# Kernel optimization log

Hardware: AMD Instinct MI355X
Metric: run time of the kernel (lower is better)

## Reference

```python
import jax, jax.numpy as jnp
import numpy as np
from jax import lax

B, C_VIS, C_GRAPH, C_OUT, H, W, K = 8, 256, 256, 256, 96, 96, 3


def conv2d(x, w, b):
    # x: [B,Cin,H,W], w: [Cout,Cin,K,K], SAME padding (pad = K//2)
    y = lax.conv_general_dilated(x, w, window_strides=(1, 1), padding='SAME',
                                 dimension_numbers=('NCHW', 'OIHW', 'NCHW'))
    return y + b[None, :, None, None]


def setup_inputs() -> dict:
    key = jax.random.key(0)
    ks = jax.random.split(key, 12)
    scale_v = 1.0 / np.sqrt(C_VIS * K * K)
    scale_g = 1.0 / np.sqrt(C_GRAPH * K * K)
    scale_o = 1.0 / np.sqrt(C_OUT * K * K)
    return {
        'feats': jax.random.normal(ks[0], (B, C_VIS, H, W), jnp.float32),
        'graph_feature': jax.random.normal(ks[1], (B, C_GRAPH, H, W), jnp.float32),
        'wq': jax.random.normal(ks[2], (C_OUT, C_GRAPH, K, K), jnp.float32) * scale_g,
        'bq': jax.random.normal(ks[3], (C_OUT,), jnp.float32) * 0.01,
        'wk': jax.random.normal(ks[4], (C_OUT, C_VIS, K, K), jnp.float32) * scale_v,
        'bk': jax.random.normal(ks[5], (C_OUT,), jnp.float32) * 0.01,
        'wv': jax.random.normal(ks[6], (C_OUT, C_VIS, K, K), jnp.float32) * scale_v,
        'bv': jax.random.normal(ks[7], (C_OUT,), jnp.float32) * 0.01,
        'wo': jax.random.normal(ks[8], (C_OUT, C_OUT, K, K), jnp.float32) * scale_o,
        'bo': jax.random.normal(ks[9], (C_OUT,), jnp.float32) * 0.01,
    }


def reference(feats, graph_feature, wq, bq, wk, bk, wv, bv, wo, bo):
    q = conv2d(graph_feature, wq, bq)  # [B,C,H,W]
    k = conv2d(feats, wk, bk)          # [B,C,H,W]
    v = conv2d(feats, wv, bv)          # [B,C,H,W]
    # attention over rows: attn[b,c,i,j] = sum_w q[b,c,i,w] * k[b,c,j,w]
    scale = 1.0 / jnp.sqrt(jnp.asarray(k.shape[-1], q.dtype))
    attn = jnp.einsum('bchw,bcgw->bchg', q, k) * scale  # [B,C,H,H]
    attn = jax.nn.softmax(attn, axis=-1)
    fused = jnp.einsum('bchg,bcgw->bchw', attn, v)      # [B,C,H,W]
    return conv2d(fused, wo, bo)
```

## Files before the change

kernel.cpp:

```cpp
#include <hip/hip_runtime.h>
#include <hip/hip_bf16.h>

constexpr int BATCH = 8;
constexpr int CH    = 256;
constexpr int H     = 96;
constexpr int W     = 96;
constexpr int HW    = H * W;
constexpr long PLANE_ELEMS = (long)BATCH * CH * HW;
constexpr int PAD   = 98;

typedef short  bf16x8_t  __attribute__((ext_vector_type(8)));
typedef float  f32x4_t   __attribute__((ext_vector_type(4)));
typedef float  f32x16_t  __attribute__((ext_vector_type(16)));

__device__ inline uint pk2_bf16(float a, float b) {
  ushort lo = __bfloat16_as_ushort(__float2bfloat16(a));
  ushort hi = __bfloat16_as_ushort(__float2bfloat16(b));
  return (uint)lo | ((uint)hi << 16);
}

#define WAITVM(N) asm volatile("s_waitcnt vmcnt(" #N ")" ::: "memory")

__device__ __forceinline__ void gl_lds16(const ushort* g, ushort* l) {
  __builtin_amdgcn_global_load_lds(
      (const __attribute__((address_space(1))) void*)g,
      (__attribute__((address_space(3))) void*)l, 16, 0, 0);
}

__global__ __launch_bounds__(256) void prep_wb(
    const float* __restrict__ s0, const float* __restrict__ s1,
    const float* __restrict__ s2, const float* __restrict__ s3,
    ushort* __restrict__ d0, ushort* __restrict__ d1,
    ushort* __restrict__ d2, ushort* __restrict__ d3,
    ushort* __restrict__ p0, ushort* __restrict__ p1)
{
  if (blockIdx.x < 9216) {
    const int t = blockIdx.x / 2304;
    const int idx = (blockIdx.x % 2304) * 256 + threadIdx.x;
    const float* s = (t == 0) ? s0 : (t == 1) ? s1 : (t == 2) ? s2 : s3;
    ushort* d      = (t == 0) ? d0 : (t == 1) ? d1 : (t == 2) ? d2 : d3;
    const int e    = idx & 7;
    const int lane = (idx >> 3) & 63;
    const int kh   = (idx >> 9) & 1;
    const int q32  = (idx >> 10) & 7;
    const int cc   = (idx >> 13) & 7;
    const int tap  = idx >> 16;
    const int co   = q32 * 32 + (lane & 31);
    const int ci   = cc * 32 + kh * 16 + (lane >> 5) * 8 + e;
    d[idx] = __bfloat16_as_ushort(__float2bfloat16(s[(co * 256 + ci) * 9 + tap]));
    return;
  }
  const int bb = blockIdx.x - 9216;
  const int ub = bb % 49;
  const int b  = (bb / 49) & 7;
  ushort* p = (bb >= 392) ? p1 : p0;
  const int u = ub * 256 + threadIdx.x;
  if (u >= 12416) return;
  int y, x, cu;
  if (u < 6272)      { y = (u < 3136) ? 0 : 97; int r = u % 3136; x = r >> 5; cu = r & 31; }
  else               { int r = u - 6272; x = (r < 3072) ? 0 : 97; int r2 = r % 3072; y = 1 + (r2 >> 5); cu = r2 & 31; }
  int4 z = make_int4(0, 0, 0, 0);
  *(int4*)&p[(((long)b * PAD + y) * PAD + x) * 256 + cu * 8] = z;
}

__global__ __launch_bounds__(256) void nchw_f32_to_nhwc_bf16_2(
    const float* __restrict__ in0, const float* __restrict__ in1,
    ushort* __restrict__ out0, ushort* __restrict__ out1)
{
  __shared__ float t[32][33];
  const int tid = threadIdx.x;
  const int p0 = blockIdx.x * 32;
  const int c0 = blockIdx.y * 32;
  const int ts = blockIdx.z >> 3;
  const int b  = blockIdx.z & 7;
  const float* in = ts ? in1 : in0;
  ushort* out     = ts ? out1 : out0;
  const int tp = tid & 31, tc8 = tid >> 5;
#pragma unroll
  for (int i = 0; i < 4; ++i) {
    int c = tc8 + i * 8;
    t[c][tp] = in[((long)(b * 256 + c0 + c)) * HW + p0 + tp];
  }
  __syncthreads();
  const int wc = tid & 31, wp8 = tid >> 5;
#pragma unroll
  for (int i = 0; i < 4; ++i) {
    int p = p0 + wp8 + i * 8;
    int y = p / 96, x = p % 96;
    out[(((long)b * PAD + y + 1) * PAD + x + 1) * 256 + c0 + wc] =
        __bfloat16_as_ushort(__float2bfloat16(t[wc][wp8 + i * 8]));
  }
}

__global__ __launch_bounds__(256) void nchw_bf16_to_nhwc_bf16(
    const ushort* __restrict__ in, ushort* __restrict__ out)
{
  __shared__ ushort t[32][34];
  const int tid = threadIdx.x;
  const int p0 = blockIdx.x * 32;
  const int c0 = blockIdx.y * 32;
  const int b  = blockIdx.z;
  const int tp = tid & 31, tc8 = tid >> 5;
#pragma unroll
  for (int i = 0; i < 4; ++i) {
    int c = tc8 + i * 8;
    t[c][tp] = in[((long)(b * 256 + c0 + c)) * HW + p0 + tp];
  }
  __syncthreads();
  const int wc = tid & 31, wp8 = tid >> 5;
#pragma unroll
  for (int i = 0; i < 4; ++i) {
    int p = p0 + wp8 + i * 8;
    int y = p / 96, x = p % 96;
    out[(((long)b * PAD + y + 1) * PAD + x + 1) * 256 + c0 + wc] = t[wc][wp8 + i * 8];
  }
}

template <int NT, typename OutT>
__global__ __launch_bounds__(256, 2) void conv3x3_mfma(
    const ushort* pin0, const ushort* pin1,
    const ushort* w0, const ushort* w1, const ushort* w2,
    const float* bias0, const float* bias1, const float* bias2,
    OutT* o0, OutT* o1, OutT* o2)
{
  const int tid  = threadIdx.x;
  const int lane = tid & 63;
  const int wv   = tid >> 6;
  const int wm   = wv & 1;
  const int wn   = wv >> 1;
  const int l31  = lane & 31;
  const int hi   = lane >> 5;

  const int nwg = NT * 768;
  const int cpx = nwg >> 3;
  const int swz = ((int)blockIdx.x & 7) * cpx + ((int)blockIdx.x >> 3);
  const int t    = swz / 768;
  const int rest = swz % 768;
  const ushort* pin = (t == 2) ? pin1 : pin0;
  const ushort* wt  = (t == 0) ? w0 : (t == 1) ? w1 : w2;
  const float* bias = (t == 0) ? bias0 : (t == 1) ? bias1 : bias2;
  OutT* out         = (t == 0) ? o0 : (t == 1) ? o1 : o2;

  const int cox = rest & 1;
  const int yb  = (rest >> 1) % 48;
  const int b   = (rest >> 1) / 48;
  const int co0 = cox * 128;
  const int y0  = yb * 2;
  const int q32b = cox * 4 + wm * 2;

  __shared__ ushort sIn[2][1568 * 8];

  f32x16_t acc[2][3];
#pragma unroll
  for (int ct = 0; ct < 2; ++ct)
#pragma unroll
    for (int pt = 0; pt < 3; ++pt)
#pragma unroll
      for (int e = 0; e < 16; ++e) acc[ct][pt][e] = 0.f;

  auto issueIN = [&](int cc) {
    const int ci0 = cc * 32;
    const int ubase = wv * 392;
#pragma unroll
    for (int it = 0; it < 7; ++it) {
      int lo = it * 64 + lane;
      if (lo < 392) {
        int u  = ubase + lo;
        int q  = u >> 2;
        int g  = u & 3;
        int xx = q % 98, rr = q / 98;
        int ug = g ^ ((xx + (xx >> 2)) & 3);
        const ushort* src = pin + (((long)(b * PAD + y0 + rr)) * PAD + xx) * 256 + ci0 + ug * 8;
        ushort* dst = (ushort*)((char*)&sIn[cc & 1][0] + (long)u * 16);
        gl_lds16(src, dst);
      }
    }
  };

  auto glda = [&](int tap, int cc, int f) -> bf16x8_t {
    return *(const bf16x8_t*)&wt[((((tap * 8 + cc) * 8 + q32b + (f >> 1)) * 2
                                   + (f & 1)) << 9) + (lane << 3)];
  };

  bf16x8_t a0[4], a1[4], a2[4];

#define ISSUE_A(CC, TAP, AR)                \
  if ((CC) < 8) {                           \
    AR[0] = glda((TAP), (CC), 0);           \
    AR[1] = glda((TAP), (CC), 1);           \
    AR[2] = glda((TAP), (CC), 2);           \
    AR[3] = glda((TAP), (CC), 3);           \
  }

  auto dotap = [&](int DY, int DX, int bi, const bf16x8_t* a) {
    bf16x8_t bb[6];
    const char* Bb = (const char*)&sIn[bi][0];
    const int rr   = wn + DY;
#pragma unroll
    for (int pt = 0; pt < 3; ++pt) {
      const int s = pt * 32 + l31 + DX;
      const int sw = (s + (s >> 2)) & 3;
#pragma unroll
      for (int kh = 0; kh < 2; ++kh) {
        const int g = ((kh << 1) | hi) ^ sw;
        bb[pt * 2 + kh] = *(const bf16x8_t*)(Bb + ((rr * 98 + s) << 6) + (g << 4));
      }
    }
    __builtin_amdgcn_s_setprio(1);
#pragma unroll
    for (int kh = 0; kh < 2; ++kh)
#pragma unroll
      for (int ct = 0; ct < 2; ++ct)
#pragma unroll
        for (int pt = 0; pt < 3; ++pt)
          acc[ct][pt] = __builtin_amdgcn_mfma_f32_32x32x16_bf16(
              a[ct * 2 + kh], bb[pt * 2 + kh], acc[ct][pt], 0, 0, 0);
    __builtin_amdgcn_s_setprio(0);
  };

  issueIN(0);
  __builtin_amdgcn_sched_barrier(0);
  ISSUE_A(0, 0, a0);
  ISSUE_A(0, 1, a1);
  __builtin_amdgcn_sched_barrier(0);
  WAITVM(8);
  __builtin_amdgcn_s_barrier();
  __builtin_amdgcn_sched_barrier(0);

#pragma unroll 1
  for (int c = 0; c < 8; ++c) {
    const int bi = c & 1;
    if (c < 7) issueIN(c + 1);
    __builtin_amdgcn_sched_barrier(0);
    ISSUE_A(c, 2, a2)  dotap(0, 0, bi, a0);
    ISSUE_A(c, 3, a0)  dotap(0, 1, bi, a1);
    ISSUE_A(c, 4, a1)  dotap(0, 2, bi, a2);
    ISSUE_A(c, 5, a2)  dotap(1, 0, bi, a0);
    ISSUE_A(c, 6, a0)  dotap(1, 1, bi, a1);
    ISSUE_A(c, 7, a1)  dotap(1, 2, bi, a2);
    ISSUE_A(c, 8, a2)  dotap(2, 0, bi, a0);
    ISSUE_A(c + 1, 0, a0)  dotap(2, 1, bi, a1);
    ISSUE_A(c + 1, 1, a1)  dotap(2, 2, bi, a2);
    __builtin_amdgcn_sched_barrier(0);
    if (c < 7) { WAITVM(36); } else { WAITVM(0); }
    __builtin_amdgcn_s_barrier();
    __builtin_amdgcn_sched_barrier(0);
  }
#undef ISSUE_A

  if constexpr (sizeof(OutT) == 2) {
    char* sE = (char*)&sIn[0][0];
#pragma unroll
    for (int h = 0; h < 2; ++h) {
      if (wm == h) {
#pragma unroll
        for (int ct = 0; ct < 2; ++ct)
#pragma unroll
          for (int r = 0; r < 16; ++r) {
            const int col = ct * 32 + (r & 3) + 8 * (r >> 2) + 4 * hi;
            const float bv = bias[co0 + h * 64 + col];
#pragma unroll
            for (int pt = 0; pt < 3; ++pt) {
              *(ushort*)(sE + col * 400 + (wn * 96 + pt * 32 + l31) * 2) =
                  __bfloat16_as_ushort(__float2bfloat16(acc[ct][pt][r] + bv));
            }
          }
      }
      __syncthreads();
#pragma unroll
      for (int it = 0; it < 7; ++it) {
        int u = it * 256 + tid;
        if (u < 1600) {
          int co = u / 25, ru = u % 25;
          if (ru < 24) {
            int4 v = *(const int4*)(sE + co * 400 + ru * 16);
            int e0 = ru * 8;
            int yy = y0 + (e0 >= 96);
            int x  = e0 - (e0 >= 96 ? 96 : 0);
            *(int4*)&out[(((long)(b * 256 + co0 + h * 64 + co)) * 96 + yy) * 96 + x] = v;
          }
        }
      }
      __syncthreads();
    }
  } else {
    char* sE = (char*)&sIn[0][0];
#pragma unroll
    for (int h = 0; h < 2; ++h) {
      if (wm == h) {
#pragma unroll
        for (int ct = 0; ct < 2; ++ct)
#pragma unroll
          for (int r = 0; r < 16; ++r) {
            const int col = ct * 32 + (r & 3) + 8 * (r >> 2) + 4 * hi;
            const float bv = bias[co0 + h * 64 + col];
#pragma unroll
            for (int pt = 0; pt < 3; ++pt) {
              *(float*)(sE + (col * 196 + wn * 96 + pt * 32 + l31) * 4) =
                  acc[ct][pt][r] + bv;
            }
          }
      }
      __syncthreads();
#pragma unroll
      for (int it = 0; it < 12; ++it) {
        int u = it * 256 + tid;
        int co = u / 48, ru = u % 48;
        int4 v = *(const int4*)(sE + (co * 196 + ru * 4) * 4);
        int e0 = ru * 4;
        int yy = y0 + (e0 >= 96);
        int x  = e0 - (e0 >= 96 ? 96 : 0);
        *(int4*)&out[(((long)(b * 256 + co0 + h * 64 + co)) * 96 + yy) * 96 + x] = v;
      }
      __syncthreads();
    }
  }
}

constexpr int APITCH = 104;

__global__ __launch_bounds__(384, 3) void attn_mfma(
    const ushort* __restrict__ q,
    const ushort* __restrict__ k,
    const ushort* __restrict__ v,
    ushort* __restrict__ outf)
{
  __shared__ ushort sK [96 * APITCH];
  __shared__ ushort sVt[96 * APITCH];
  __shared__ ushort sP [6 * 16 * APITCH];

  const int tid  = threadIdx.x;
  const int lane = tid & 63;
  const int wv   = tid >> 6;
  const int l15  = lane & 15;
  const int lg   = lane >> 4;
  const long plane = (long)blockIdx.x * HW;

  for (int u = tid; u < 1152; u += 384) {
    int j = u / 12, c8 = u % 12;
    *(int4*)&sK[j * APITCH + c8 * 8] = *(const int4*)&k[plane + j * 96 + c8 * 8];
  }
  for (int u = tid; u < 1152; u += 384) {
    int j = u % 96, c8 = u / 96;
    ushort tmp[8];
    *(int4*)tmp = *(const int4*)&v[plane + j * 96 + c8 * 8];
#pragma unroll
    for (int e = 0; e < 8; ++e)
      sVt[(c8 * 8 + e) * APITCH + j] = tmp[e];
  }
  __syncthreads();

  const int i0 = wv * 16;

  bf16x8_t qf[3];
#pragma unroll
  for (int ks = 0; ks < 3; ++ks)
    qf[ks] = *(const bf16x8_t*)&q[plane + (i0 + l15) * 96 + ks * 32 + lg * 8];

  f32x4_t s[6];
#pragma unroll
  for (int jt = 0; jt < 6; ++jt) s[jt] = (f32x4_t){0.f, 0.f, 0.f, 0.f};
#pragma unroll
  for (int jt = 0; jt < 6; ++jt)
#pragma unroll
    for (int ks = 0; ks < 3; ++ks) {
      bf16x8_t kf = *(const bf16x8_t*)&sK[(jt * 16 + l15) * APITCH + ks * 32 + lg * 8];
      s[jt] = __builtin_amdgcn_mfma_f32_16x16x32_bf16(kf, qf[ks], s[jt], 0, 0, 0);
    }

  const float sc = 0.10206207261596575f;
  float m = -3.0e38f;
#pragma unroll
  for (int jt = 0; jt < 6; ++jt)
#pragma unroll
    for (int r = 0; r < 4; ++r) m = fmaxf(m, s[jt][r]);
  m = fmaxf(m, __shfl_xor(m, 16));
  m = fmaxf(m, __shfl_xor(m, 32));

  float p[6][4];
  float sum = 0.f;
#pragma unroll
  for (int jt = 0; jt < 6; ++jt)
#pragma unroll
    for (int r = 0; r < 4; ++r) {
      float e = __expf((s[jt][r] - m) * sc);
      p[jt][r] = e;
      sum += e;
    }
  sum += __shfl_xor(sum, 16);
  sum += __shfl_xor(sum, 32);
  const float inv = 1.f / sum;

  ushort* myP = &sP[wv * 16 * APITCH];
#pragma unroll
  for (int jt = 0; jt < 6; ++jt) {
    *(uint*)&myP[l15 * APITCH + jt * 16 + lg * 4] =
        pk2_bf16(p[jt][0] * inv, p[jt][1] * inv);
    *(uint*)&myP[l15 * APITCH + jt * 16 + lg * 4 + 2] =
        pk2_bf16(p[jt][2] * inv, p[jt][3] * inv);
  }

  bf16x8_t pf[3];
#pragma unroll
  for (int ks = 0; ks < 3; ++ks)
    pf[ks] = *(const bf16x8_t*)&myP[l15 * APITCH + ks * 32 + lg * 8];

  f32x4_t o[6];
#pragma unroll
  for (int wt = 0; wt < 6; ++wt) o[wt] = (f32x4_t){0.f, 0.f, 0.f, 0.f};
#pragma unroll
  for (int wt = 0; wt < 6; ++wt)
#pragma unroll
    for (int ks = 0; ks < 3; ++ks) {
      bf16x8_t vf = *(const bf16x8_t*)&sVt[(wt * 16 + l15) * APITCH + ks * 32 + lg * 8];
      o[wt] = __builtin_amdgcn_mfma_f32_16x16x32_bf16(pf[ks], vf, o[wt], 0, 0, 0);
    }

#pragma unroll
  for (int wt = 0; wt < 6; ++wt)
#pragma unroll
    for (int r = 0; r < 4; ++r) {
      int i = i0 + lg * 4 + r;
      outf[plane + i * 96 + wt * 16 + l15] =
          __bfloat16_as_ushort(__float2bfloat16(o[wt][r]));
    }
}

extern "C" void kernel_launch(void* const* d_in, const int* in_sizes, int n_in,
                              void* d_out, int out_size, void* d_ws, size_t ws_size,
                              hipStream_t stream) {
  (void)in_sizes; (void)n_in; (void)out_size; (void)ws_size;

  const float* feats = (const float*)d_in[0];
  const float* graph = (const float*)d_in[1];
  const float* wq    = (const float*)d_in[2];
  const float* bq    = (const float*)d_in[3];
  const float* wk    = (const float*)d_in[4];
  const float* bk    = (const float*)d_in[5];
  const float* wv    = (const float*)d_in[6];
  const float* bv    = (const float*)d_in[7];
  const float* wo    = (const float*)d_in[8];
  const float* bo    = (const float*)d_in[9];
  float* out = (float*)d_out;

  char* ws = (char*)d_ws;
  const long planeB   = PLANE_ELEMS * 2;
  const long pinElems = (long)BATCH * PAD * PAD * 256;
  ushort* qb   = (ushort*)ws;
  ushort* kb   = (ushort*)(ws + planeB);
  ushort* vb   = (ushort*)(ws + 2 * planeB);
  ushort* pinF = (ushort*)(ws + 3 * planeB);
  ushort* pinG = pinF + pinElems;
  ushort* wtq  = pinG + pinElems;
  ushort* wtk  = wtq + 9 * 256 * 256;
  ushort* wtv  = wtk + 9 * 256 * 256;
  ushort* wto  = wtv + 9 * 256 * 256;

  dim3 tgrid2(HW / 32, CH / 32, 2 * BATCH);
  dim3 tgrid (HW / 32, CH / 32, BATCH);
  dim3 agrid (BATCH * CH);

  prep_wb<<<9216 + 784, 256, 0, stream>>>(wq, wk, wv, wo, wtq, wtk, wtv, wto,
                                          pinF, pinG);

  nchw_f32_to_nhwc_bf16_2<<<tgrid2, 256, 0, stream>>>(feats, graph, pinF, pinG);

  conv3x3_mfma<3, ushort><<<3 * 768, 256, 0, stream>>>(
      pinF, pinG, wtk, wtv, wtq, bk, bv, bq, kb, vb, qb);

  attn_mfma<<<agrid, 384, 0, stream>>>(qb, kb, vb, qb);

  nchw_bf16_to_nhwc_bf16<<<tgrid, 256, 0, stream>>>(qb, pinF);

  conv3x3_mfma<1, float><<<768, 256, 0, stream>>>(
      pinF, pinF, wto, wto, wto, bo, bo, bo, out, out, out);
}
```

Before: 416.9 us.

## Split conv3x3 output channels across 8 waves with 512-thread blocks

```diff
diff --git a/kernel.cpp b/kernel.cpp
--- a/kernel.cpp
+++ b/kernel.cpp
@@ -117,7 +117,7 @@
 }
 
 template <int NT, typename OutT>
-__global__ __launch_bounds__(256, 2) void conv3x3_mfma(
+__global__ __launch_bounds__(512, 4) void conv3x3_mfma(
     const ushort* pin0, const ushort* pin1,
     const ushort* w0, const ushort* w1, const ushort* w2,
     const float* bias0, const float* bias1, const float* bias2,
@@ -126,8 +126,8 @@
   const int tid  = threadIdx.x;
   const int lane = tid & 63;
   const int wv   = tid >> 6;
-  const int wm   = wv & 1;
-  const int wn   = wv >> 1;
+  const int wm   = wv & 3;
+  const int wn   = wv >> 2;
   const int l31  = lane & 31;
   const int hi   = lane >> 5;
 
@@ -146,25 +146,23 @@
   const int b   = (rest >> 1) / 48;
   const int co0 = cox * 128;
   const int y0  = yb * 2;
-  const int q32b = cox * 4 + wm * 2;
+  const int q32b = cox * 4 + wm;
 
   __shared__ ushort sIn[2][1568 * 8];
 
-  f32x16_t acc[2][3];
-#pragma unroll
-  for (int ct = 0; ct < 2; ++ct)
-#pragma unroll
-    for (int pt = 0; pt < 3; ++pt)
-#pragma unroll
-      for (int e = 0; e < 16; ++e) acc[ct][pt][e] = 0.f;
+  f32x16_t acc[3];
+#pragma unroll
+  for (int pt = 0; pt < 3; ++pt)
+#pragma unroll
+    for (int e = 0; e < 16; ++e) acc[pt][e] = 0.f;
 
   auto issueIN = [&](int cc) {
     const int ci0 = cc * 32;
-    const int ubase = wv * 392;
-#pragma unroll
-    for (int it = 0; it < 7; ++it) {
+    const int ubase = wv * 196;
+#pragma unroll
+    for (int it = 0; it < 4; ++it) {
       int lo = it * 64 + lane;
-      if (lo < 392) {
+      if (lo < 196) {
         int u  = ubase + lo;
         int q  = u >> 2;
         int g  = u & 3;
@@ -177,19 +175,17 @@
     }
   };
 
-  auto glda = [&](int tap, int cc, int f) -> bf16x8_t {
-    return *(const bf16x8_t*)&wt[((((tap * 8 + cc) * 8 + q32b + (f >> 1)) * 2
-                                   + (f & 1)) << 9) + (lane << 3)];
+  auto glda = [&](int tap, int cc, int kh) -> bf16x8_t {
+    return *(const bf16x8_t*)&wt[((((tap * 8 + cc) * 8 + q32b) * 2 + kh) << 9)
+                                 + (lane << 3)];
   };
 
-  bf16x8_t a0[4], a1[4], a2[4];
+  bf16x8_t a0[2], a1[2], a2[2];
 
 #define ISSUE_A(CC, TAP, AR)                \
   if ((CC) < 8) {                           \
     AR[0] = glda((TAP), (CC), 0);           \
     AR[1] = glda((TAP), (CC), 1);           \
-    AR[2] = glda((TAP), (CC), 2);           \
-    AR[3] = glda((TAP), (CC), 3);           \
   }
 
   auto dotap = [&](int DY, int DX, int bi, const bf16x8_t* a) {
@@ -210,11 +206,9 @@
 #pragma unroll
     for (int kh = 0; kh < 2; ++kh)
 #pragma unroll
-      for (int ct = 0; ct < 2; ++ct)
-#pragma unroll
-        for (int pt = 0; pt < 3; ++pt)
-          acc[ct][pt] = __builtin_amdgcn_mfma_f32_32x32x16_bf16(
-              a[ct * 2 + kh], bb[pt * 2 + kh], acc[ct][pt], 0, 0, 0);
+      for (int pt = 0; pt < 3; ++pt)
+        acc[pt] = __builtin_amdgcn_mfma_f32_32x32x16_bf16(
+            a[kh], bb[pt * 2 + kh], acc[pt], 0, 0, 0);
     __builtin_amdgcn_s_setprio(0);
   };
 
@@ -223,7 +217,7 @@
   ISSUE_A(0, 0, a0);
   ISSUE_A(0, 1, a1);
   __builtin_amdgcn_sched_barrier(0);
-  WAITVM(8);
+  WAITVM(4);
   __builtin_amdgcn_s_barrier();
   __builtin_amdgcn_sched_barrier(0);
 
@@ -242,7 +236,7 @@
     ISSUE_A(c + 1, 0, a0)  dotap(2, 1, bi, a1);
     ISSUE_A(c + 1, 1, a1)  dotap(2, 2, bi, a2);
     __builtin_amdgcn_sched_barrier(0);
-    if (c < 7) { WAITVM(36); } else { WAITVM(0); }
+    if (c < 7) { WAITVM(18); } else { WAITVM(0); }
     __builtin_amdgcn_s_barrier();
     __builtin_amdgcn_sched_barrier(0);
   }
@@ -251,60 +245,46 @@
   if constexpr (sizeof(OutT) == 2) {
     char* sE = (char*)&sIn[0][0];
 #pragma unroll
+    for (int r = 0; r < 16; ++r) {
+      const int col = wm * 32 + (r & 3) + 8 * (r >> 2) + 4 * hi;
+      const float bv = bias[co0 + col];
+#pragma unroll
+      for (int pt = 0; pt < 3; ++pt) {
+        *(ushort*)(sE + col * 392 + (wn * 96 + pt * 32 + l31) * 2) =
+            __bfloat16_as_ushort(__float2bfloat16(acc[pt][r] + bv));
+      }
+    }
+    __syncthreads();
+#pragma unroll
+    for (int it = 0; it < 6; ++it) {
+      int u = it * 512 + tid;
+      int co = u / 24, ru = u % 24;
+      int4 v = *(const int4*)(sE + co * 392 + ru * 16);
+      int e0 = ru * 8;
+      int yy = y0 + (e0 >= 96);
+      int x  = e0 - (e0 >= 96 ? 96 : 0);
+      *(int4*)&out[(((long)(b * 256 + co0 + co)) * 96 + yy) * 96 + x] = v;
+    }
+  } else {
+    char* sE = (char*)&sIn[0][0];
+#pragma unroll
     for (int h = 0; h < 2; ++h) {
-      if (wm == h) {
-#pragma unroll
-        for (int ct = 0; ct < 2; ++ct)
-#pragma unroll
-          for (int r = 0; r < 16; ++r) {
-            const int col = ct * 32 + (r & 3) + 8 * (r >> 2) + 4 * hi;
-            const float bv = bias[co0 + h * 64 + col];
-#pragma unroll
-            for (int pt = 0; pt < 3; ++pt) {
-              *(ushort*)(sE + col * 400 + (wn * 96 + pt * 32 + l31) * 2) =
-                  __bfloat16_as_ushort(__float2bfloat16(acc[ct][pt][r] + bv));
-            }
-          }
-      }
-      __syncthreads();
-#pragma unroll
-      for (int it = 0; it < 7; ++it) {
-        int u = it * 256 + tid;
-        if (u < 1600) {
-          int co = u / 25, ru = u % 25;
-          if (ru < 24) {
-            int4 v = *(const int4*)(sE + co * 400 + ru * 16);
-            int e0 = ru * 8;
-            int yy = y0 + (e0 >= 96);
-            int x  = e0 - (e0 >= 96 ? 96 : 0);
-            *(int4*)&out[(((long)(b * 256 + co0 + h * 64 + co)) * 96 + yy) * 96 + x] = v;
+      if ((wm >> 1) == h) {
+#pragma unroll
+        for (int r = 0; r < 16; ++r) {
+          const int col = (wm & 1) * 32 + (r & 3) + 8 * (r >> 2) + 4 * hi;
+          const float bv = bias[co0 + h * 64 + col];
+#pragma unroll
+          for (int pt = 0; pt < 3; ++pt) {
+            *(float*)(sE + (col * 196 + wn * 96 + pt * 32 + l31) * 4) =
+                acc[pt][r] + bv;
           }
         }
       }
       __syncthreads();
-    }
-  } else {
-    char* sE = (char*)&sIn[0][0];
-#pragma unroll
-    for (int h = 0; h < 2; ++h) {
-      if (wm == h) {
-#pragma unroll
-        for (int ct = 0; ct < 2; ++ct)
-#pragma unroll
-          for (int r = 0; r < 16; ++r) {
-            const int col = ct * 32 + (r & 3) + 8 * (r >> 2) + 4 * hi;
-            const float bv = bias[co0 + h * 64 + col];
-#pragma unroll
-            for (int pt = 0; pt < 3; ++pt) {
-              *(float*)(sE + (col * 196 + wn * 96 + pt * 32 + l31) * 4) =
-                  acc[ct][pt][r] + bv;
-            }
-          }
-      }
-      __syncthreads();
-#pragma unroll
-      for (int it = 0; it < 12; ++it) {
-        int u = it * 256 + tid;
+#pragma unroll
+      for (int it = 0; it < 6; ++it) {
+        int u = it * 512 + tid;
         int co = u / 48, ru = u % 48;
         int4 v = *(const int4*)(sE + (co * 196 + ru * 4) * 4);
         int e0 = ru * 4;
@@ -465,13 +445,13 @@
 
   nchw_f32_to_nhwc_bf16_2<<<tgrid2, 256, 0, stream>>>(feats, graph, pinF, pinG);
 
-  conv3x3_mfma<3, ushort><<<3 * 768, 256, 0, stream>>>(
+  conv3x3_mfma<3, ushort><<<3 * 768, 512, 0, stream>>>(
       pinF, pinG, wtk, wtv, wtq, bk, bv, bq, kb, vb, qb);
 
   attn_mfma<<<agrid, 384, 0, stream>>>(qb, kb, vb, qb);
 
   nchw_bf16_to_nhwc_bf16<<<tgrid, 256, 0, stream>>>(qb, pinF);
 
-  conv3x3_mfma<1, float><<<768, 256, 0, stream>>>(
+  conv3x3_mfma<1, float><<<768, 512, 0, stream>>>(
       pinF, pinF, wto, wto, wto, bo, bo, bo, out, out, out);
 }
```

Measured after the change: 555.3 us. 33.2% more time.
